# Performance work log

Measured on AMD Instinct MI355X. Metric: run time of the kernel, lower is better.

Reference implementation:

```python
import jax, jax.numpy as jnp
import numpy as np

N_HEAD = 16


def setup_inputs() -> dict:
    key = jax.random.key(0)
    ks = jax.random.split(key, 5)
    B, T, C = 4, 2048, 1024
    # torch Linear stored as [out,in]; we use [in,out] so x @ W matches x @ W_t.T
    return {
        "x": jax.random.normal(ks[0], (B, T, C), jnp.float32),
        "c_attn_w": jax.random.normal(ks[1], (C, 3 * C), jnp.float32) * 0.02,
        "c_attn_b": jax.random.normal(ks[2], (3 * C,), jnp.float32) * 0.02,
        "c_proj_w": jax.random.normal(ks[3], (C, C), jnp.float32) * 0.02,
        "c_proj_b": jax.random.normal(ks[4], (C,), jnp.float32) * 0.02,
    }


def reference(x, c_attn_w, c_attn_b, c_proj_w, c_proj_b):
    B, T, C = x.shape
    H = N_HEAD
    d = C // H
    qkv = x @ c_attn_w + c_attn_b                      # [B,T,3C]
    q, k, v = jnp.split(qkv, 3, axis=2)
    q = q.reshape(B, T, H, d).transpose(0, 2, 1, 3)    # [B,H,T,d]
    k = k.reshape(B, T, H, d).transpose(0, 2, 1, 3)
    v = v.reshape(B, T, H, d).transpose(0, 2, 1, 3)
    scale = 1.0 / jnp.sqrt(jnp.asarray(d, x.dtype))
    w = jnp.einsum("bhqd,bhkd->bhqk", q, k) * scale    # [B,H,T,T]
    causal = jnp.tril(jnp.ones((T, T), bool))
    w = jnp.where(causal, w, jnp.asarray(-jnp.inf, w.dtype))
    w = jax.nn.softmax(w, axis=-1)
    y = jnp.einsum("bhqk,bhkd->bhqd", w, v)            # [B,H,T,d]
    y = y.transpose(0, 2, 1, 3).reshape(B, T, C)
    return y @ c_proj_w + c_proj_b
```

## Files before the change

kernel.cpp:

```cpp
#include <hip/hip_runtime.h>
#include <hip/hip_bf16.h>
#include <stdint.h>

#define DEV __device__ __forceinline__

typedef __attribute__((ext_vector_type(8))) short short8;
typedef __attribute__((ext_vector_type(8))) _Float16 half8;
typedef __attribute__((ext_vector_type(2))) __fp16 fp16x2;
typedef __attribute__((ext_vector_type(16))) float floatx16;

#if __has_builtin(__builtin_amdgcn_exp2f)
#define EXP2F __builtin_amdgcn_exp2f
#else
#define EXP2F exp2f
#endif

DEV unsigned short f2bf(float f) {
  union { float f; uint32_t u; } v; v.f = f;
  uint32_t u = v.u;
  u += 0x7fffu + ((u >> 16) & 1u);
  return (unsigned short)(u >> 16);
}
DEV unsigned short f2h(float f) {
  union { _Float16 h; unsigned short u; } c; c.h = (_Float16)f; return c.u;
}
DEV void async_cp16(const unsigned short* g, unsigned short* l) {
  __builtin_amdgcn_global_load_lds(
      (const __attribute__((address_space(1))) uint32_t*)g,
      (__attribute__((address_space(3))) uint32_t*)l, 16, 0, 0);
}

__global__ __launch_bounds__(256)
void cvt_x_kernel(const float* __restrict__ x, unsigned short* __restrict__ xb) {
  const size_t i = ((size_t)blockIdx.x * 256 + threadIdx.x) * 4;
  const float4 f = *(const float4*)(x + i);
  ushort4 w;
  w.x = f2bf(f.x); w.y = f2bf(f.y); w.z = f2bf(f.z); w.w = f2bf(f.w);
  *(ushort4*)(xb + i) = w;
}

__global__ __launch_bounds__(256)
void transpose_w_kernel(const float* __restrict__ W, unsigned short* __restrict__ Wt,
                        int K, int N) {
  __shared__ float tile[64][65];
  const int k0 = blockIdx.y * 64, n0 = blockIdx.x * 64;
  const int tr = threadIdx.x >> 4;
  const int tc = (threadIdx.x & 15) * 4;
#pragma unroll
  for (int it = 0; it < 4; ++it) {
    const int k = tr + it * 16;
    const float4 f = *(const float4*)(W + (size_t)(k0 + k) * N + n0 + tc);
    tile[k][tc + 0] = f.x; tile[k][tc + 1] = f.y;
    tile[k][tc + 2] = f.z; tile[k][tc + 3] = f.w;
  }
  __syncthreads();
#pragma unroll
  for (int it = 0; it < 4; ++it) {
    const int n = tr + it * 16;
    ushort4 w;
    w.x = f2bf(tile[tc + 0][n]); w.y = f2bf(tile[tc + 1][n]);
    w.z = f2bf(tile[tc + 2][n]); w.w = f2bf(tile[tc + 3][n]);
    *(ushort4*)(Wt + (size_t)(n0 + n) * K + k0 + tc) = w;
  }
}

template <int EPI>
__global__ __launch_bounds__(256)
void gemm_bt_kernel(const unsigned short* __restrict__ A,
                    const unsigned short* __restrict__ Bt,
                    const float* __restrict__ bias, int M, int N, int K,
                    unsigned short* __restrict__ qws,
                    unsigned short* __restrict__ kws,
                    unsigned short* __restrict__ vws,
                    float* __restrict__ out) {
  __shared__ __align__(16) unsigned short As[128 * 64];
  __shared__ __align__(16) unsigned short Bs[128 * 64];
  const int tid = threadIdx.x;
  const int wid = tid >> 6, lane = tid & 63;
  const int l32 = lane & 31, hf = lane >> 5;
  const int wm = wid >> 1, wn = wid & 1;
  const int rowA0 = blockIdx.y * 128;
  const int colB0 = blockIdx.x * 128;

  const unsigned short* gA[4];
  const unsigned short* gB[4];
  unsigned short* lA[4];
  unsigned short* lB[4];
#pragma unroll
  for (int it = 0; it < 4; ++it) {
    const int CI = it * 256 + tid;
    const int row = CI >> 3;
    const int c = (CI & 7) ^ (row & 7);
    gA[it] = A + (size_t)(rowA0 + row) * K + c * 8;
    gB[it] = Bt + (size_t)(colB0 + row) * K + c * 8;
    lA[it] = &As[(it * 256 + wid * 64) * 8];
    lB[it] = &Bs[(it * 256 + wid * 64) * 8];
  }

  int aoff[2][4], boff[2][4];
#pragma unroll
  for (int ti = 0; ti < 2; ++ti)
#pragma unroll
    for (int s = 0; s < 4; ++s) {
      const int ra = wm * 64 + ti * 32 + l32;
      const int rb = wn * 64 + ti * 32 + l32;
      aoff[ti][s] = ra * 64 + ((2 * s + hf) ^ (ra & 7)) * 8;
      boff[ti][s] = rb * 64 + ((2 * s + hf) ^ (rb & 7)) * 8;
    }

  floatx16 acc[2][2];
#pragma unroll
  for (int i = 0; i < 2; ++i)
#pragma unroll
    for (int j = 0; j < 2; ++j)
#pragma unroll
      for (int r = 0; r < 16; ++r) acc[i][j][r] = 0.f;

  for (int kt = 0; kt < K; kt += 64) {
    __syncthreads();
#pragma unroll
    for (int it = 0; it < 4; ++it) {
      async_cp16(gA[it] + kt, lA[it]);
      async_cp16(gB[it] + kt, lB[it]);
    }
    __syncthreads();
#pragma unroll
    for (int s = 0; s < 4; ++s) {
      const short8 a0 = *(const short8*)&As[aoff[0][s]];
      const short8 a1 = *(const short8*)&As[aoff[1][s]];
      const short8 b0 = *(const short8*)&Bs[boff[0][s]];
      const short8 b1 = *(const short8*)&Bs[boff[1][s]];
      acc[0][0] = __builtin_amdgcn_mfma_f32_32x32x16_bf16(a0, b0, acc[0][0], 0, 0, 0);
      acc[0][1] = __builtin_amdgcn_mfma_f32_32x32x16_bf16(a0, b1, acc[0][1], 0, 0, 0);
      acc[1][0] = __builtin_amdgcn_mfma_f32_32x32x16_bf16(a1, b0, acc[1][0], 0, 0, 0);
      acc[1][1] = __builtin_amdgcn_mfma_f32_32x32x16_bf16(a1, b1, acc[1][1], 0, 0, 0);
    }
  }

  constexpr float QSCALE = 0.18033688011112042f;
#pragma unroll
  for (int mi = 0; mi < 2; ++mi) {
#pragma unroll
    for (int nj = 0; nj < 2; ++nj) {
      const int col = colB0 + wn * 64 + nj * 32 + l32;
      const float bv = bias[col];
#pragma unroll
      for (int reg = 0; reg < 16; ++reg) {
        const int ri = (reg & 3) + 8 * (reg >> 2) + 4 * hf;
        const int R = rowA0 + wm * 64 + mi * 32 + ri;
        const float v = acc[mi][nj][reg] + bv;
        if constexpr (EPI == 0) {
          const int b = R >> 11, t = R & 2047;
          const int which = col >> 10, c = col & 1023;
          const int h = c >> 6, dd = c & 63;
          const size_t bh = (size_t)(b * 16 + h);
          if (which == 0)
            qws[(bh * 2048 + t) * 64 + dd] = f2bf(v * QSCALE);
          else if (which == 1)
            kws[(bh * 2048 + t) * 64 + dd] = f2bf(v);
          else
            vws[(bh * 64 + dd) * 2048 + t] = f2h(v);
        } else {
          out[(size_t)R * N + col] = v;
        }
      }
    }
  }
}

__global__ __launch_bounds__(256, 2)
void attn_mfma_kernel(const unsigned short* __restrict__ qws,
                      const unsigned short* __restrict__ kws,
                      const unsigned short* __restrict__ vws,
                      unsigned short* __restrict__ yws) {
  constexpr int T = 2048, D = 64;
  __shared__ __align__(16) unsigned short Ks[128 * 64];
  __shared__ __align__(16) unsigned short Vs[64 * 128];
  const int tid = threadIdx.x;
  const int wid = tid >> 6, lane = tid & 63;
  const int hf = lane >> 5, l32 = lane & 31;
  const int bh = blockIdx.x;
  const int qt = 15 - (int)blockIdx.y;
  const int qbase = qt * 128;
  const unsigned short* Qp = qws + (size_t)bh * T * D;
  const unsigned short* Kp = kws + (size_t)bh * T * D;
  const unsigned short* Vp = vws + (size_t)bh * D * T;

  const unsigned short* pK[4];
  const unsigned short* pV[4];
  unsigned short* lK[4];
  unsigned short* lV[4];
#pragma unroll
  for (int it = 0; it < 4; ++it) {
    const int CI = it * 256 + tid;
    const int rK = CI >> 3, cK = (CI & 7) ^ (rK & 7);
    const int rV = CI >> 4, cV = (CI & 15) ^ (rV & 15);
    pK[it] = Kp + (size_t)rK * D + cK * 8;
    pV[it] = Vp + (size_t)rV * T + cV * 8;
    lK[it] = &Ks[(it * 256 + wid * 64) * 8];
    lV[it] = &Vs[(it * 256 + wid * 64) * 8];
  }

  const int q = qbase + wid * 32 + l32;
  short8 qf[4];
#pragma unroll
  for (int s = 0; s < 4; ++s)
    qf[s] = *(const short8*)(Qp + (size_t)q * D + s * 16 + hf * 8);

  int koff[4], voff[8];
#pragma unroll
  for (int s = 0; s < 4; ++s)
    koff[s] = l32 * 64 + ((2 * s + hf) ^ (l32 & 7)) * 8;
#pragma unroll
  for (int s = 0; s < 8; ++s)
    voff[s] = l32 * 128 + ((2 * s + hf) ^ (l32 & 15)) * 8;

  floatx16 Oacc[2];
#pragma unroll
  for (int mt2 = 0; mt2 < 2; ++mt2)
#pragma unroll
    for (int i = 0; i < 16; ++i) Oacc[mt2][i] = 0.f;
  float lrun = 0.f;

  for (int kt = 0; kt <= qt; ++kt) {
    const int kb = kt * 128;
    __syncthreads();
#pragma unroll
    for (int it = 0; it < 4; ++it) {
      async_cp16(pK[it] + (size_t)kb * D, lK[it]);
      async_cp16(pV[it] + kb, lV[it]);
    }
    __syncthreads();

    const bool diag = (kt == qt);
    const int mtmax = diag ? (wid + 1) : 4;

    floatx16 S[4];
#pragma unroll
    for (int mt = 0; mt < 4; ++mt)
      if (mt < mtmax)
#pragma unroll
        for (int i = 0; i < 16; ++i) S[mt][i] = 0.f;

#pragma unroll
    for (int s = 0; s < 4; ++s) {
#pragma unroll
      for (int mt = 0; mt < 4; ++mt)
        if (mt < mtmax) {
          const short8 kf = *(const short8*)&Ks[mt * 2048 + koff[s]];
          S[mt] = __builtin_amdgcn_mfma_f32_32x32x16_bf16(kf, qf[s], S[mt], 0, 0, 0);
        }
    }

    if (diag) {
#pragma unroll
      for (int mt = 0; mt < 4; ++mt)
        if (mt == wid) {
#pragma unroll
          for (int r = 0; r < 16; ++r) {
            const int intra = (r & 3) + 8 * (r >> 2) + 4 * hf;
            if (intra > l32) S[mt][r] = -1e30f;
          }
        }
    }

    float tsum = 0.f;
    uint32_t pk[4][8];
#pragma unroll
    for (int mt = 0; mt < 4; ++mt)
      if (mt < mtmax)
#pragma unroll
        for (int t = 0; t < 8; ++t) {
          const float pa = EXP2F(S[mt][2 * t]);
          const float pb = EXP2F(S[mt][2 * t + 1]);
          tsum += pa + pb;
          union { fp16x2 h; uint32_t u; } cv;
          cv.h = __builtin_amdgcn_cvt_pkrtz(pa, pb);
          pk[mt][t] = cv.u;
        }
    tsum += __shfl_xor(tsum, 32, 64);
    lrun += tsum;

    const int smax = 2 * mtmax;
#pragma unroll
    for (int s = 0; s < 8; ++s)
      if (s < smax) {
        const int mt = s >> 1;
        const int bo = 4 * (s & 1);
        const uint32_t own0 = hf ? pk[mt][bo + 2] : pk[mt][bo];
        const uint32_t own1 = hf ? pk[mt][bo + 3] : pk[mt][bo + 1];
        const uint32_t sendA = hf ? pk[mt][bo] : pk[mt][bo + 2];
        const uint32_t sendB = hf ? pk[mt][bo + 1] : pk[mt][bo + 3];
        const uint32_t recvA = (uint32_t)__shfl_xor((int)sendA, 32, 64);
        const uint32_t recvB = (uint32_t)__shfl_xor((int)sendB, 32, 64);
        union { uint32_t u[4]; half8 h; } bb;
        bb.u[0] = hf ? recvA : own0;
        bb.u[1] = hf ? recvB : own1;
        bb.u[2] = hf ? own0 : recvA;
        bb.u[3] = hf ? own1 : recvB;
#pragma unroll
        for (int mt2 = 0; mt2 < 2; ++mt2) {
          const half8 vf = *(const half8*)&Vs[mt2 * 4096 + voff[s]];
          Oacc[mt2] = __builtin_amdgcn_mfma_f32_32x32x16_f16(vf, bb.h, Oacc[mt2], 0, 0, 0);
        }
      }
  }

  const float invl = 1.0f / lrun;
  const int b_ = bh >> 4, h_ = bh & 15;
  unsigned short* yrow = yws + ((size_t)(b_ * 2048 + q)) * 1024 + h_ * 64;
#pragma unroll
  for (int mt2 = 0; mt2 < 2; ++mt2)
#pragma unroll
    for (int t = 0; t < 8; ++t) {
      const int d0 = mt2 * 32 + 2 * (t & 1) + 8 * (t >> 1) + 4 * hf;
      const uint32_t ua = f2bf(Oacc[mt2][2 * t] * invl);
      const uint32_t ub = f2bf(Oacc[mt2][2 * t + 1] * invl);
      *(uint32_t*)&yrow[d0] = ua | (ub << 16);
    }
}

extern "C" void kernel_launch(void* const* d_in, const int* in_sizes, int n_in,
                              void* d_out, int out_size, void* d_ws, size_t ws_size,
                              hipStream_t stream) {
  (void)in_sizes; (void)n_in; (void)out_size;
  const float* x = (const float*)d_in[0];
  const float* attn_w = (const float*)d_in[1];
  const float* attn_b = (const float*)d_in[2];
  const float* proj_w = (const float*)d_in[3];
  const float* proj_b = (const float*)d_in[4];
  float* out = (float*)d_out;

  const size_t NQ = 8388608;
  unsigned short* qws = (unsigned short*)d_ws;
  unsigned short* kws = qws + NQ;
  unsigned short* vws = kws + NQ;
  unsigned short* yws = vws + NQ;
  unsigned short* xb  = yws + NQ;
  unsigned short* wta = xb + NQ;
  unsigned short* wtp = wta + 3072 * 1024;
  if (ws_size < (5 * NQ + 4 * 1024 * 1024) * sizeof(unsigned short)) return;

  cvt_x_kernel<<<dim3(8192), dim3(256), 0, stream>>>(x, xb);
  transpose_w_kernel<<<dim3(48, 16), dim3(256), 0, stream>>>(attn_w, wta, 1024, 3072);
  transpose_w_kernel<<<dim3(16, 16), dim3(256), 0, stream>>>(proj_w, wtp, 1024, 1024);

  gemm_bt_kernel<0><<<dim3(24, 64), dim3(256), 0, stream>>>(
      xb, wta, attn_b, 8192, 3072, 1024, qws, kws, vws, nullptr);
  attn_mfma_kernel<<<dim3(64, 16), dim3(256), 0, stream>>>(qws, kws, vws, yws);
  gemm_bt_kernel<1><<<dim3(8, 64), dim3(256), 0, stream>>>(
      yws, wtp, proj_b, 8192, 1024, 1024, nullptr, nullptr, nullptr, out);
}
```

Measured before the change: 291.3 us.

## Enlarge GEMM tiles to 256x128 and stage 256-key blocks in attention

The GEMM kernel now computes a 256x128 output tile per block, with each wave holding 4x2 MFMA accumulators. This reuses each B fragment across more A rows and halves the grid in M. The attention kernel loads 256 keys of K and V per barrier pair and processes them as two 128-key sub-tiles, which halves the number of __syncthreads and load phases. The cost is larger LDS use (48KB in the GEMM, 64KB in attention) and more accumulator registers, which may reduce occupancy. The smaller GEMM grids may also underfill the CUs.

Result: slower. 316.6 us (+8.7%).

```diff
diff --git a/kernel.cpp b/kernel.cpp
--- a/kernel.cpp
+++ b/kernel.cpp
@@ -73,44 +73,42 @@
                     unsigned short* __restrict__ kws,
                     unsigned short* __restrict__ vws,
                     float* __restrict__ out) {
-  __shared__ __align__(16) unsigned short As[128 * 64];
+  __shared__ __align__(16) unsigned short As[256 * 64];
   __shared__ __align__(16) unsigned short Bs[128 * 64];
   const int tid = threadIdx.x;
-  const int wid = tid >> 6, lane = tid & 63;
+  const int wid = tid >> 6;
+  const int lane = tid & 63;
   const int l32 = lane & 31, hf = lane >> 5;
   const int wm = wid >> 1, wn = wid & 1;
-  const int rowA0 = blockIdx.y * 128;
+  const int rowA0 = blockIdx.y * 256;
   const int colB0 = blockIdx.x * 128;
 
-  const unsigned short* gA[4];
-  const unsigned short* gB[4];
-  unsigned short* lA[4];
-  unsigned short* lB[4];
-#pragma unroll
-  for (int it = 0; it < 4; ++it) {
-    const int CI = it * 256 + tid;
-    const int row = CI >> 3;
-    const int c = (CI & 7) ^ (row & 7);
-    gA[it] = A + (size_t)(rowA0 + row) * K + c * 8;
-    gB[it] = Bt + (size_t)(colB0 + row) * K + c * 8;
-    lA[it] = &As[(it * 256 + wid * 64) * 8];
-    lB[it] = &Bs[(it * 256 + wid * 64) * 8];
-  }
-
-  int aoff[2][4], boff[2][4];
-#pragma unroll
-  for (int ti = 0; ti < 2; ++ti)
+  const int srow = tid >> 3;
+  const int sc = ((tid & 7) ^ (srow & 7)) * 8;
+  const unsigned short* gAb = A + (size_t)(rowA0 + srow) * K + sc;
+  const unsigned short* gBb = Bt + (size_t)(colB0 + srow) * K + sc;
+  unsigned short* lAb = &As[wid * 512];
+  unsigned short* lBb = &Bs[wid * 512];
+
+  int aoff[4][4], boff[2][4];
+#pragma unroll
+  for (int ti = 0; ti < 4; ++ti)
 #pragma unroll
     for (int s = 0; s < 4; ++s) {
-      const int ra = wm * 64 + ti * 32 + l32;
-      const int rb = wn * 64 + ti * 32 + l32;
+      const int ra = wm * 128 + ti * 32 + l32;
       aoff[ti][s] = ra * 64 + ((2 * s + hf) ^ (ra & 7)) * 8;
-      boff[ti][s] = rb * 64 + ((2 * s + hf) ^ (rb & 7)) * 8;
-    }
-
-  floatx16 acc[2][2];
-#pragma unroll
-  for (int i = 0; i < 2; ++i)
+    }
+#pragma unroll
+  for (int tj = 0; tj < 2; ++tj)
+#pragma unroll
+    for (int s = 0; s < 4; ++s) {
+      const int rb = wn * 64 + tj * 32 + l32;
+      boff[tj][s] = rb * 64 + ((2 * s + hf) ^ (rb & 7)) * 8;
+    }
+
+  floatx16 acc[4][2];
+#pragma unroll
+  for (int i = 0; i < 4; ++i)
 #pragma unroll
     for (int j = 0; j < 2; ++j)
 #pragma unroll
@@ -119,27 +117,28 @@
   for (int kt = 0; kt < K; kt += 64) {
     __syncthreads();
 #pragma unroll
-    for (int it = 0; it < 4; ++it) {
-      async_cp16(gA[it] + kt, lA[it]);
-      async_cp16(gB[it] + kt, lB[it]);
-    }
+    for (int it = 0; it < 8; ++it)
+      async_cp16(gAb + (size_t)it * 32 * K + kt, lAb + it * 2048);
+#pragma unroll
+    for (int it = 0; it < 4; ++it)
+      async_cp16(gBb + (size_t)it * 32 * K + kt, lBb + it * 2048);
     __syncthreads();
 #pragma unroll
     for (int s = 0; s < 4; ++s) {
-      const short8 a0 = *(const short8*)&As[aoff[0][s]];
-      const short8 a1 = *(const short8*)&As[aoff[1][s]];
       const short8 b0 = *(const short8*)&Bs[boff[0][s]];
       const short8 b1 = *(const short8*)&Bs[boff[1][s]];
-      acc[0][0] = __builtin_amdgcn_mfma_f32_32x32x16_bf16(a0, b0, acc[0][0], 0, 0, 0);
-      acc[0][1] = __builtin_amdgcn_mfma_f32_32x32x16_bf16(a0, b1, acc[0][1], 0, 0, 0);
-      acc[1][0] = __builtin_amdgcn_mfma_f32_32x32x16_bf16(a1, b0, acc[1][0], 0, 0, 0);
-      acc[1][1] = __builtin_amdgcn_mfma_f32_32x32x16_bf16(a1, b1, acc[1][1], 0, 0, 0);
+#pragma unroll
+      for (int ti = 0; ti < 4; ++ti) {
+        const short8 a = *(const short8*)&As[aoff[ti][s]];
+        acc[ti][0] = __builtin_amdgcn_mfma_f32_32x32x16_bf16(a, b0, acc[ti][0], 0, 0, 0);
+        acc[ti][1] = __builtin_amdgcn_mfma_f32_32x32x16_bf16(a, b1, acc[ti][1], 0, 0, 0);
+      }
     }
   }
 
   constexpr float QSCALE = 0.18033688011112042f;
 #pragma unroll
-  for (int mi = 0; mi < 2; ++mi) {
+  for (int ti = 0; ti < 4; ++ti) {
 #pragma unroll
     for (int nj = 0; nj < 2; ++nj) {
       const int col = colB0 + wn * 64 + nj * 32 + l32;
@@ -147,8 +146,8 @@
 #pragma unroll
       for (int reg = 0; reg < 16; ++reg) {
         const int ri = (reg & 3) + 8 * (reg >> 2) + 4 * hf;
-        const int R = rowA0 + wm * 64 + mi * 32 + ri;
-        const float v = acc[mi][nj][reg] + bv;
+        const int R = rowA0 + wm * 128 + ti * 32 + ri;
+        const float v = acc[ti][nj][reg] + bv;
         if constexpr (EPI == 0) {
           const int b = R >> 11, t = R & 2047;
           const int which = col >> 10, c = col & 1023;
@@ -174,8 +173,8 @@
                       const unsigned short* __restrict__ vws,
                       unsigned short* __restrict__ yws) {
   constexpr int T = 2048, D = 64;
-  __shared__ __align__(16) unsigned short Ks[128 * 64];
-  __shared__ __align__(16) unsigned short Vs[64 * 128];
+  __shared__ __align__(16) unsigned short Ks[256 * 64];
+  __shared__ __align__(16) unsigned short Vs[2 * 64 * 128];
   const int tid = threadIdx.x;
   const int wid = tid >> 6, lane = tid & 63;
   const int hf = lane >> 5, l32 = lane & 31;
@@ -186,20 +185,15 @@
   const unsigned short* Kp = kws + (size_t)bh * T * D;
   const unsigned short* Vp = vws + (size_t)bh * D * T;
 
-  const unsigned short* pK[4];
-  const unsigned short* pV[4];
-  unsigned short* lK[4];
-  unsigned short* lV[4];
-#pragma unroll
-  for (int it = 0; it < 4; ++it) {
-    const int CI = it * 256 + tid;
-    const int rK = CI >> 3, cK = (CI & 7) ^ (rK & 7);
-    const int rV = CI >> 4, cV = (CI & 15) ^ (rV & 15);
-    pK[it] = Kp + (size_t)rK * D + cK * 8;
-    pV[it] = Vp + (size_t)rV * T + cV * 8;
-    lK[it] = &Ks[(it * 256 + wid * 64) * 8];
-    lV[it] = &Vs[(it * 256 + wid * 64) * 8];
-  }
+  const int srowK = tid >> 3;
+  const int scK = ((tid & 7) ^ ((tid >> 3) & 7)) * 8;
+  const unsigned short* gKb = Kp + (size_t)srowK * D + scK;
+  unsigned short* lKb = &Ks[wid * 512];
+
+  const int vd = tid >> 4;
+  const int vkc = ((tid & 15) ^ vd) * 8;
+  const unsigned short* gVb = Vp + (size_t)vd * T + vkc;
+  unsigned short* lVb = &Vs[wid * 512];
 
   const int q = qbase + wid * 32 + l32;
   short8 qf[4];
@@ -222,88 +216,98 @@
     for (int i = 0; i < 16; ++i) Oacc[mt2][i] = 0.f;
   float lrun = 0.f;
 
-  for (int kt = 0; kt <= qt; ++kt) {
-    const int kb = kt * 128;
+  const int kmax = (qt + 1) * 128;
+  const int nkb = (qt + 2) >> 1;
+  for (int kb2 = 0; kb2 < nkb; ++kb2) {
+    const int kb = kb2 * 256;
     __syncthreads();
 #pragma unroll
-    for (int it = 0; it < 4; ++it) {
-      async_cp16(pK[it] + (size_t)kb * D, lK[it]);
-      async_cp16(pV[it] + kb, lV[it]);
-    }
+    for (int it = 0; it < 8; ++it)
+      async_cp16(gKb + (size_t)(kb + it * 32) * D, lKb + it * 2048);
+#pragma unroll
+    for (int it = 0; it < 8; ++it)
+      async_cp16(gVb + (size_t)(it & 3) * 16 * T + (it >> 2) * 128 + kb,
+                 lVb + it * 2048);
     __syncthreads();
 
-    const bool diag = (kt == qt);
-    const int mtmax = diag ? (wid + 1) : 4;
-
-    floatx16 S[4];
-#pragma unroll
-    for (int mt = 0; mt < 4; ++mt)
-      if (mt < mtmax)
-#pragma unroll
-        for (int i = 0; i < 16; ++i) S[mt][i] = 0.f;
-
-#pragma unroll
-    for (int s = 0; s < 4; ++s) {
+#pragma unroll
+    for (int sb = 0; sb < 2; ++sb) {
+      const int kbs = kb + sb * 128;
+      if (kbs >= kmax) break;
+      const bool diag = (kbs == qbase);
+      const int mtmax = diag ? (wid + 1) : 4;
+
+      floatx16 S[4];
 #pragma unroll
       for (int mt = 0; mt < 4; ++mt)
-        if (mt < mtmax) {
-          const short8 kf = *(const short8*)&Ks[mt * 2048 + koff[s]];
-          S[mt] = __builtin_amdgcn_mfma_f32_32x32x16_bf16(kf, qf[s], S[mt], 0, 0, 0);
-        }
-    }
-
-    if (diag) {
+        if (mt < mtmax)
+#pragma unroll
+          for (int i = 0; i < 16; ++i) S[mt][i] = 0.f;
+
+#pragma unroll
+      for (int s = 0; s < 4; ++s) {
+#pragma unroll
+        for (int mt = 0; mt < 4; ++mt)
+          if (mt < mtmax) {
+            const short8 kf = *(const short8*)&Ks[sb * 8192 + mt * 2048 + koff[s]];
+            S[mt] = __builtin_amdgcn_mfma_f32_32x32x16_bf16(kf, qf[s], S[mt], 0, 0, 0);
+          }
+      }
+
+      if (diag) {
+#pragma unroll
+        for (int mt = 0; mt < 4; ++mt)
+          if (mt == wid) {
+#pragma unroll
+            for (int r = 0; r < 16; ++r) {
+              const int intra = (r & 3) + 8 * (r >> 2) + 4 * hf;
+              if (intra > l32) S[mt][r] = -1e30f;
+            }
+          }
+      }
+
+      float tsum = 0.f;
+      uint32_t pk[4][8];
 #pragma unroll
       for (int mt = 0; mt < 4; ++mt)
-        if (mt == wid) {
-#pragma unroll
-          for (int r = 0; r < 16; ++r) {
-            const int intra = (r & 3) + 8 * (r >> 2) + 4 * hf;
-            if (intra > l32) S[mt][r] = -1e30f;
+        if (mt < mtmax)
+#pragma unroll
+          for (int t = 0; t < 8; ++t) {
+            const float pa = EXP2F(S[mt][2 * t]);
+            const float pb = EXP2F(S[mt][2 * t + 1]);
+            tsum += pa + pb;
+            union { fp16x2 h; uint32_t u; } cv;
+            cv.h = __builtin_amdgcn_cvt_pkrtz(pa, pb);
+            pk[mt][t] = cv.u;
+          }
+      tsum += __shfl_xor(tsum, 32, 64);
+      lrun += tsum;
+
+      const int smax = 2 * mtmax;
+#pragma unroll
+      for (int s = 0; s < 8; ++s)
+        if (s < smax) {
+          const int mt = s >> 1;
+          const int bo = 4 * (s & 1);
+          const uint32_t own0 = hf ? pk[mt][bo + 2] : pk[mt][bo];
+          const uint32_t own1 = hf ? pk[mt][bo + 3] : pk[mt][bo + 1];
+          const uint32_t sendA = hf ? pk[mt][bo] : pk[mt][bo + 2];
+          const uint32_t sendB = hf ? pk[mt][bo + 1] : pk[mt][bo + 3];
+          const uint32_t recvA = (uint32_t)__shfl_xor((int)sendA, 32, 64);
+          const uint32_t recvB = (uint32_t)__shfl_xor((int)sendB, 32, 64);
+          union { uint32_t u[4]; half8 h; } bb;
+          bb.u[0] = hf ? recvA : own0;
+          bb.u[1] = hf ? recvB : own1;
+          bb.u[2] = hf ? own0 : recvA;
+          bb.u[3] = hf ? own1 : recvB;
+#pragma unroll
+          for (int mt2 = 0; mt2 < 2; ++mt2) {
+            const half8 vf = *(const half8*)&Vs[sb * 8192 + mt2 * 4096 + voff[s]];
+            Oacc[mt2] =
+                __builtin_amdgcn_mfma_f32_32x32x16_f16(vf, bb.h, Oacc[mt2], 0, 0, 0);
           }
         }
     }
-
-    float tsum = 0.f;
-    uint32_t pk[4][8];
-#pragma unroll
-    for (int mt = 0; mt < 4; ++mt)
-      if (mt < mtmax)
-#pragma unroll
-        for (int t = 0; t < 8; ++t) {
-          const float pa = EXP2F(S[mt][2 * t]);
-          const float pb = EXP2F(S[mt][2 * t + 1]);
-          tsum += pa + pb;
-          union { fp16x2 h; uint32_t u; } cv;
-          cv.h = __builtin_amdgcn_cvt_pkrtz(pa, pb);
-          pk[mt][t] = cv.u;
-        }
-    tsum += __shfl_xor(tsum, 32, 64);
-    lrun += tsum;
-
-    const int smax = 2 * mtmax;
-#pragma unroll
-    for (int s = 0; s < 8; ++s)
-      if (s < smax) {
-        const int mt = s >> 1;
-        const int bo = 4 * (s & 1);
-        const uint32_t own0 = hf ? pk[mt][bo + 2] : pk[mt][bo];
-        const uint32_t own1 = hf ? pk[mt][bo + 3] : pk[mt][bo + 1];
-        const uint32_t sendA = hf ? pk[mt][bo] : pk[mt][bo + 2];
-        const uint32_t sendB = hf ? pk[mt][bo + 1] : pk[mt][bo + 3];
-        const uint32_t recvA = (uint32_t)__shfl_xor((int)sendA, 32, 64);
-        const uint32_t recvB = (uint32_t)__shfl_xor((int)sendB, 32, 64);
-        union { uint32_t u[4]; half8 h; } bb;
-        bb.u[0] = hf ? recvA : own0;
-        bb.u[1] = hf ? recvB : own1;
-        bb.u[2] = hf ? own0 : recvA;
-        bb.u[3] = hf ? own1 : recvB;
-#pragma unroll
-        for (int mt2 = 0; mt2 < 2; ++mt2) {
-          const half8 vf = *(const half8*)&Vs[mt2 * 4096 + voff[s]];
-          Oacc[mt2] = __builtin_amdgcn_mfma_f32_32x32x16_f16(vf, bb.h, Oacc[mt2], 0, 0, 0);
-        }
-      }
   }
 
   const float invl = 1.0f / lrun;
@@ -345,9 +349,9 @@
   transpose_w_kernel<<<dim3(48, 16), dim3(256), 0, stream>>>(attn_w, wta, 1024, 3072);
   transpose_w_kernel<<<dim3(16, 16), dim3(256), 0, stream>>>(proj_w, wtp, 1024, 1024);
 
-  gemm_bt_kernel<0><<<dim3(24, 64), dim3(256), 0, stream>>>(
+  gemm_bt_kernel<0><<<dim3(24, 32), dim3(256), 0, stream>>>(
       xb, wta, attn_b, 8192, 3072, 1024, qws, kws, vws, nullptr);
   attn_mfma_kernel<<<dim3(64, 16), dim3(256), 0, stream>>>(qws, kws, vws, yws);
-  gemm_bt_kernel<1><<<dim3(8, 64), dim3(256), 0, stream>>>(
+  gemm_bt_kernel<1><<<dim3(8, 32), dim3(256), 0, stream>>>(
       yws, wtp, proj_b, 8192, 1024, 1024, nullptr, nullptr, nullptr, out);
 }
```
